# Optimization experiments

Hardware: AMD Instinct MI355X
Metric: run time of the kernel (lower is better)

## Reference

```python
import jax, jax.numpy as jnp
import numpy as np
from jax.tree_util import tree_map

B, T, D = 2, 4096, 1024
C = 512            # chunk_size
P = 16             # n_persistent
H = 2048           # neural-memory hidden
FFN = 4 * D        # ffn_mult * d_model
LR, BETA, ALPHA = 0.01, 0.9, 0.01   # memory lr / momentum / decay
EPS_LN = 1e-5


def _l2norm(x):
    n = jnp.sqrt(jnp.sum(x * x, axis=-1, keepdims=True))
    return x / jnp.maximum(n, 1e-12)


def _ln(x, g, b):
    m = jnp.mean(x, axis=-1, keepdims=True)
    v = jnp.mean((x - m) ** 2, axis=-1, keepdims=True)
    return (x - m) * jax.lax.rsqrt(v + EPS_LN) * g + b


def _mem_mlp(mem, x):
    h = jax.nn.silu(x @ mem['w0'] + mem['b0'])
    return h @ mem['w1'] + mem['b1']


def setup_inputs() -> dict:
    key = jax.random.key(0)
    ks = iter(jax.random.split(key, 32))
    w = lambda *s: jax.random.normal(next(ks), s, jnp.float32) * 0.02
    return dict(
        x=jax.random.normal(next(ks), (B, T, D), jnp.float32),
        wq_ctx=w(D, D), wq=w(D, D), wk=w(D, D), wv=w(D, D),
        w_attn_out=w(D, D), w_gate=w(D, D),
        gate_g=jnp.ones(D), gate_b=jnp.zeros(D),
        n1_g=jnp.ones(D), n1_b=jnp.zeros(D),
        n2_g=jnp.ones(D), n2_b=jnp.zeros(D),
        ffn_w1=w(D, FFN), ffn_b1=jnp.zeros(FFN),
        ffn_w2=w(FFN, D), ffn_b2=jnp.zeros(D),
        pers=w(P, D),
        mem_w0=w(D, H), mem_b0=jnp.zeros(H),
        mem_w1=w(H, D), mem_b1=jnp.zeros(D),
        mem_wk=w(D, D), mem_wv=w(D, D),
    )


def reference(x, wq_ctx, wq, wk, wv, w_attn_out, w_gate, gate_g, gate_b,
              n1_g, n1_b, n2_g, n2_b, ffn_w1, ffn_b1, ffn_w2, ffn_b2,
              pers, mem_w0, mem_b0, mem_w1, mem_b1, mem_wk, mem_wv):
    Bv, Tv, Dv = x.shape
    n_chunks = Tv // C
    scale = Dv ** 0.5
    S = P + 2 * C   # persistent + retrieved-memory tokens + segment
    # prefix-aware causal mask: i attends to j if j < P (persistent prefix) or j <= i
    ii = jnp.arange(S)[:, None]
    jj = jnp.arange(S)[None, :]
    mask = (jj < P) | (jj <= ii)                      # (S, S)

    mem0 = dict(w0=mem_w0, b0=mem_b0, w1=mem_w1, b1=mem_b1)
    mom0 = tree_map(jnp.zeros_like, mem0)

    def attn(seq):                                    # cosine causal attention, single head
        q = _l2norm(seq @ wq) * scale
        k = _l2norm(seq @ wk)
        v = seq @ wv
        scores = jnp.einsum('bqd,bkd->bqk', q, k)
        scores = jnp.where(mask, scores, -jnp.inf)
        a = jax.nn.softmax(scores, axis=-1)
        return jnp.einsum('bqk,bkd->bqd', a, v) @ w_attn_out

    def step(carry, seg):                             # seg: (B, C, D)
        mem, mom = carry
        h = _mem_mlp(mem, _l2norm(seg @ wq_ctx))      # memory retrieval, (B, C, D)
        aug = jnp.concatenate(
            [jnp.broadcast_to(pers, (Bv, P, Dv)), h, seg], axis=1)  # (B, S, D)
        y_aug = aug + attn(_ln(aug, n1_g, n1_b))
        y_t = y_aug[:, P + C:, :]                     # strip persistent, keep last C

        # surprise-gradient memory update with momentum + decay
        kk = y_t @ mem_wk
        vv = y_t @ mem_wv
        loss = lambda m: 0.5 * jnp.sum((_mem_mlp(m, kk) - vv) ** 2) / (Bv * C)
        g = jax.grad(loss)(mem)
        mom = tree_map(lambda m_, g_: BETA * m_ + g_, mom, g)
        mem = tree_map(lambda p_, m_: (1.0 - ALPHA) * p_ - LR * m_, mem, mom)

        mem_out = _mem_mlp(mem, _l2norm(y_t @ wq_ctx))
        gate = jax.nn.sigmoid(_ln(y_t, gate_g, gate_b) @ w_gate)
        o = y_t * gate + mem_out * (1.0 - gate)
        h2 = _ln(o, n2_g, n2_b)
        o = o + (jax.nn.silu(h2 @ ffn_w1 + ffn_b1) @ ffn_w2 + ffn_b2)
        return (mem, mom), o

    x_chunks = x.reshape(Bv, n_chunks, C, Dv).transpose(1, 0, 2, 3)
    _, outs = jax.lax.scan(step, (mem0, mom0), x_chunks)   # (n_chunks, B, C, D)
    return outs.transpose(1, 0, 2, 3).reshape(Bv, Tv, Dv)
```

## Files before the change

### kernel.cpp

```cpp
#include <hip/hip_runtime.h>

#define DD 1024
#define HH 2048
#define TT 4096
#define CC 512
#define PPc 16
#define SB 1040
#define KA 1088
#define FFd 4096
#define NCH 8

typedef _Float16 f16x8 __attribute__((ext_vector_type(8)));
typedef float f32x4 __attribute__((ext_vector_type(4)));

typedef const __attribute__((address_space(1))) _Float16* gas_t;
typedef __attribute__((address_space(3))) _Float16* las_t;

__device__ __forceinline__ void async_cp16(const _Float16* g, _Float16* l) {
    __builtin_amdgcn_global_load_lds((gas_t)g, (las_t)l, 16, 0, 0);
}

template<int N> __device__ __forceinline__ void waitvm() {
    static_assert(N == 0 || N == 2 || N == 3 || N == 4 || N == 6 || N == 8, "unsupported vmcnt");
    if constexpr (N == 0)      asm volatile("s_waitcnt vmcnt(0)" ::: "memory");
    else if constexpr (N == 2) asm volatile("s_waitcnt vmcnt(2)" ::: "memory");
    else if constexpr (N == 3) asm volatile("s_waitcnt vmcnt(3)" ::: "memory");
    else if constexpr (N == 4) asm volatile("s_waitcnt vmcnt(4)" ::: "memory");
    else if constexpr (N == 6) asm volatile("s_waitcnt vmcnt(6)" ::: "memory");
    else                       asm volatile("s_waitcnt vmcnt(8)" ::: "memory");
}
#define BARRIER() asm volatile("s_barrier" ::: "memory")

struct GP {
    const _Float16* A; long bsA;
    const _Float16* Bt; long bsB;
    const float* bias;
    const float* resid; long ldr, bsR;
    const float* aux;   long ldx, bsX;
    float* Cf; long ldc, bsC;
    _Float16* Ch; long ldh, bsH;
    _Float16* Ct; long ldt, bsT;
    float* Mom;
    float* Cf2;
    float s1, s2;
    int M, N, K, act;
};

template<int BM, int BN>
__global__ __launch_bounds__(256) void gemm16(GP g)
{
    constexpr int WM = BM / 2, WN = BN / 2;
    constexpr int FA = WM / 16, FB = WN / 16;
    constexpr int LA = BM / 32, LB = BN / 32;
    constexpr int LL = LA + LB;
    constexpr int APAN = BM * 64, BPAN = BN * 64;
    constexpr int NB = 3;
    __shared__ _Float16 smem[NB * (APAN + BPAN)];
    const int tid = threadIdx.x;

    const int gx = gridDim.x, gy = gridDim.y;
    const int nwg = gx * gy * (int)gridDim.z;
    const int orig = ((int)blockIdx.z * gy + (int)blockIdx.y) * gx + (int)blockIdx.x;
    const int xcd = orig & 7, loc = orig >> 3;
    const int q8 = nwg >> 3, r8 = nwg & 7;
    const int lid = (xcd < r8 ? xcd * (q8 + 1) : r8 * (q8 + 1) + (xcd - r8) * q8) + loc;
    const int bxi = lid % gx;
    const int rem = lid / gx;
    const int byi = rem % gy;
    const int z = rem / gy;

    const int K = g.K;
    const int m0 = byi * BM, n0 = bxi * BN;
    const _Float16* Ab = g.A + (long)z * g.bsA + (long)m0 * K;
    const _Float16* Bb = g.Bt + (long)z * g.bsB + (long)n0 * K;
    const int wave = tid >> 6, lane = tid & 63;
    const int wr = wave >> 1, wc = wave & 1;
    const int fr = lane & 15, kq = lane >> 4;
    const int srow = tid >> 3;
    const int sc8 = (((tid & 7) ^ (srow & 7)) << 3);
    f32x4 acc[FA][FB] = {};

    auto stage = [&](int q, int kk) {
#pragma unroll
        for (int r = 0; r < LA; ++r)
            async_cp16(Ab + (long)(r * 32 + srow) * K + kk + sc8,
                       &smem[q * APAN + r * 2048 + wave * 512]);
#pragma unroll
        for (int r = 0; r < LB; ++r)
            async_cp16(Bb + (long)(r * 32 + srow) * K + kk + sc8,
                       &smem[NB * APAN + q * BPAN + r * 2048 + wave * 512]);
    };

    const int sl0 = ((kq ^ (fr & 7)) << 3);
    const int sl1 = (((4 + kq) ^ (fr & 7)) << 3);

    auto compute = [&](int q) {
        f16x8 af[2][FA], bf[2][FB];
        const int abase = q * APAN;
#pragma unroll
        for (int i = 0; i < FA; ++i) {
            const int ro = (wr * WM + i * 16 + fr) * 64;
            af[0][i] = *(const f16x8*)&smem[abase + ro + sl0];
            af[1][i] = *(const f16x8*)&smem[abase + ro + sl1];
        }
        const int bbase = NB * APAN + q * BPAN;
#pragma unroll
        for (int j = 0; j < FB; ++j) {
            const int ro = (wc * WN + j * 16 + fr) * 64;
            bf[0][j] = *(const f16x8*)&smem[bbase + ro + sl0];
            bf[1][j] = *(const f16x8*)&smem[bbase + ro + sl1];
        }
        __builtin_amdgcn_s_setprio(1);
#pragma unroll
        for (int h = 0; h < 2; ++h)
#pragma unroll
            for (int i = 0; i < FA; ++i)
#pragma unroll
                for (int j = 0; j < FB; ++j)
                    acc[i][j] = __builtin_amdgcn_mfma_f32_16x16x32_f16(af[h][i], bf[h][j], acc[i][j], 0, 0, 0);
        __builtin_amdgcn_s_setprio(0);
    };

    const int nk = K >> 6;
    stage(0, 0); stage(1, 64);
    int qc = 0, qs = 2;
    for (int t = 0; t < nk; ++t) {
        if (t + 1 < nk) waitvm<LL>(); else waitvm<0>();
        BARRIER();
        if (t + 2 < nk) stage(qs, (t + 2) << 6);
        compute(qc);
        qc = (qc == NB - 1) ? 0 : qc + 1;
        qs = (qs == NB - 1) ? 0 : qs + 1;
    }

#pragma unroll
    for (int i = 0; i < FA; ++i) {
        const int gm0 = m0 + wr * WM + i * 16 + kq * 4;
#pragma unroll
        for (int j = 0; j < FB; ++j) {
            const int gn = n0 + wc * WN + j * 16 + fr;
            if (gn >= g.N) continue;
            if (g.act == 4) {
                const int seg = gn >> 10, gl = gn & 1023;
#pragma unroll
                for (int r = 0; r < 4; ++r) {
                    const int gm = gm0 + r;
                    if (gm >= g.M) continue;
                    const float v = acc[i][j][r];
                    if (seg == 0) g.Ch[(long)gm * 1024 + gl] = (_Float16)v;
                    else if (seg == 1) g.Cf[(long)gm * 1024 + gl] = v;
                    else g.Cf2[(long)gm * 1024 + gl] = v;
                }
            } else {
                const float bv = g.bias ? g.bias[gn] : 0.f;
#pragma unroll
                for (int r = 0; r < 4; ++r) {
                    const int gm = gm0 + r;
                    if (gm >= g.M) continue;
                    const float raw = acc[i][j][r] + bv;
                    float av = raw;
                    if (g.act == 1) av = raw / (1.f + __expf(-raw));
                    else if (g.act == 2) {
                        const float a = g.aux[(long)z * g.bsX + (long)gm * g.ldx + gn];
                        const float s = 1.f / (1.f + __expf(-a));
                        av = raw * (s * (1.f + a * (1.f - s)));
                    }
                    float v = g.s1 * av;
                    if (g.resid) v += g.s2 * g.resid[(long)z * g.bsR + (long)gm * g.ldr + gn];
                    if (g.Cf) g.Cf[(long)z * g.bsC + (long)gm * g.ldc + gn] = (g.act == 1) ? raw : v;
                    if (g.Ch) g.Ch[(long)z * g.bsH + (long)gm * g.ldh + gn] = (_Float16)v;
                    acc[i][j][r] = v;
                }
            }
        }
    }

    if (g.Ct && (g.act != 4 || n0 < 1024)) {
        constexpr int TP = BM + 8;
        __syncthreads();
#pragma unroll
        for (int i = 0; i < FA; ++i) {
            const int lm = wr * WM + i * 16 + kq * 4;
#pragma unroll
            for (int j = 0; j < FB; ++j) {
                const int ln = wc * WN + j * 16 + fr;
#pragma unroll
                for (int r = 0; r < 4; ++r)
                    smem[ln * TP + lm + r] = (_Float16)acc[i][j][r];
            }
        }
        __syncthreads();
        constexpr int TPC = 256 / BN;
        constexpr int SEG = BM / TPC;
        const int ln = tid / TPC, part = tid % TPC;
        const int gn = n0 + ln;
        if (gn < g.N) {
            const int gmb = m0 + part * SEG;
            _Float16* dst = g.Ct + (long)z * g.bsT + (long)gn * g.ldt + gmb;
            const _Float16* src = &smem[ln * TP + part * SEG];
#pragma unroll
            for (int gi = 0; gi < SEG / 8; ++gi)
                if (gmb + gi * 8 < g.M)
                    *(uint4*)(dst + gi * 8) = *(const uint4*)(src + gi * 8);
        }
    }
}

__global__ void momupT_k(const float* __restrict__ dW1, float* __restrict__ mom1,
                         float* __restrict__ w1m, _Float16* __restrict__ w1row,
                         _Float16* __restrict__ w1t,
                         const float* __restrict__ dW0, float* __restrict__ mom0,
                         float* __restrict__ w0m, _Float16* __restrict__ w0t)
{
    __shared__ _Float16 t[64][65];
    const int b = blockIdx.x;
    const int tid = threadIdx.x;
    const float* dW; float* mom; float* wm; _Float16* wrow; _Float16* wT;
    int C, RT, r0, c0;
    if (b < 512) {
        dW = dW1; mom = mom1; wm = w1m; wrow = w1row; wT = w1t;
        C = 1024; RT = 2048;
        r0 = (b >> 4) << 6; c0 = (b & 15) << 6;
    } else {
        const int bb = b - 512;
        dW = dW0; mom = mom0; wm = w0m; wrow = nullptr; wT = w0t;
        C = 2048; RT = 1024;
        r0 = (bb >> 5) << 6; c0 = (bb & 31) << 6;
    }
#pragma unroll
    for (int i = 0; i < 4; ++i) {
        const int f = i * 256 + tid;
        const int rr = f >> 4;
        const int c4 = (f & 15) << 2;
        const long idx = (long)(r0 + rr) * C + c0 + c4;
        const float4 d = *(const float4*)(dW + idx);
        float4 mo = *(const float4*)(mom + idx);
        float4 w  = *(const float4*)(wm + idx);
        mo.x = 0.9f * mo.x + d.x; mo.y = 0.9f * mo.y + d.y;
        mo.z = 0.9f * mo.z + d.z; mo.w = 0.9f * mo.w + d.w;
        w.x = 0.99f * w.x - 0.01f * mo.x; w.y = 0.99f * w.y - 0.01f * mo.y;
        w.z = 0.99f * w.z - 0.01f * mo.z; w.w = 0.99f * w.w - 0.01f * mo.w;
        *(float4*)(mom + idx) = mo;
        *(float4*)(wm + idx) = w;
        const _Float16 h0 = (_Float16)w.x, h1 = (_Float16)w.y,
                       h2 = (_Float16)w.z, h3 = (_Float16)w.w;
        if (wrow) {
            wrow[idx] = h0; wrow[idx + 1] = h1;
            wrow[idx + 2] = h2; wrow[idx + 3] = h3;
        }
        t[rr][c4] = h0; t[rr][c4 + 1] = h1; t[rr][c4 + 2] = h2; t[rr][c4 + 3] = h3;
    }
    __syncthreads();
#pragma unroll
    for (int i = 0; i < 4; ++i) {
        const int f = i * 256 + tid;
        const int cc = f >> 4;
        const int rr4 = (f & 15) << 2;
        ushort4 u;
        u.x = *(const unsigned short*)&t[rr4][cc];
        u.y = *(const unsigned short*)&t[rr4 + 1][cc];
        u.z = *(const unsigned short*)&t[rr4 + 2][cc];
        u.w = *(const unsigned short*)&t[rr4 + 3][cc];
        *(ushort4*)(wT + (long)(c0 + cc) * RT + r0 + rr4) = u;
    }
}

__global__ void cvt_k(const float* __restrict__ in, _Float16* __restrict__ out, long n)
{
    long i = ((long)blockIdx.x * 256 + threadIdx.x) * 4;
    if (i >= n) return;
    const float4 v = *(const float4*)(in + i);
    out[i] = (_Float16)v.x; out[i + 1] = (_Float16)v.y;
    out[i + 2] = (_Float16)v.z; out[i + 3] = (_Float16)v.w;
}

__global__ void cvtT_k(const float* __restrict__ in, _Float16* __restrict__ out, int R, int C)
{
    __shared__ _Float16 t[64][65];
    const int c0 = blockIdx.x * 64, r0 = blockIdx.y * 64;
    const int tid = threadIdx.x;
    for (int i = 0; i < 16; ++i) {
        const int lin = i * 256 + tid;
        const int r = lin >> 6, cc = lin & 63;
        t[r][cc] = (_Float16)in[(long)(r0 + r) * C + c0 + cc];
    }
    __syncthreads();
    for (int i = 0; i < 16; ++i) {
        const int lin = i * 256 + tid;
        const int r2 = lin >> 6, c2 = lin & 63;
        out[(long)(c0 + r2) * R + r0 + c2] = t[c2][r2];
    }
}

__global__ void l2n16s_k(const float* __restrict__ in, long ld,
                         _Float16* __restrict__ out, float scale)
{
    const long row = blockIdx.x;
    const float* p = in + row * ld;
    _Float16* q = out + row * DD;
    const int t = threadIdx.x;
    float e0 = p[t], e1 = p[t + 256], e2 = p[t + 512], e3 = p[t + 768];
    __shared__ float rq[256];
    rq[t] = e0 * e0 + e1 * e1 + e2 * e2 + e3 * e3;
    __syncthreads();
    for (int k = 128; k; k >>= 1) { if (t < k) rq[t] += rq[t + k]; __syncthreads(); }
    const float f = scale / fmaxf(sqrtf(rq[0]), 1e-12f);
    q[t] = (_Float16)(e0 * f); q[t + 256] = (_Float16)(e1 * f);
    q[t + 512] = (_Float16)(e2 * f); q[t + 768] = (_Float16)(e3 * f);
}

__global__ void l2qk_k(const float* __restrict__ qk, _Float16* __restrict__ q16,
                       _Float16* __restrict__ k16)
{
    const int blk = blockIdx.x;
    const float* p; _Float16* o; float scale;
    if (blk < 1024) {
        const int b = blk >> 9, r = blk & 511;
        p = qk + (long)(b * SB + PPc + CC + r) * 2048;
        o = q16 + (long)blk * DD; scale = 32.f;
    } else {
        const int row = blk - 1024;
        p = qk + (long)row * 2048 + 1024;
        o = k16 + (long)row * DD; scale = 1.f;
    }
    const int t = threadIdx.x;
    float e0 = p[t], e1 = p[t + 256], e2 = p[t + 512], e3 = p[t + 768];
    __shared__ float rq[256];
    rq[t] = e0 * e0 + e1 * e1 + e2 * e2 + e3 * e3;
    __syncthreads();
    for (int k = 128; k; k >>= 1) { if (t < k) rq[t] += rq[t + k]; __syncthreads(); }
    const float f = scale / fmaxf(sqrtf(rq[0]), 1e-12f);
    o[t] = (_Float16)(e0 * f); o[t + 256] = (_Float16)(e1 * f);
    o[t + 512] = (_Float16)(e2 * f); o[t + 768] = (_Float16)(e3 * f);
}

__global__ void ln16_k(const float* __restrict__ x, const float* __restrict__ g,
                       const float* __restrict__ b, _Float16* __restrict__ o)
{
    const long row = blockIdx.x;
    const float* p = x + row * DD;
    _Float16* q = o + row * DD;
    const int t = threadIdx.x;
    float e0 = p[t], e1 = p[t + 256], e2 = p[t + 512], e3 = p[t + 768];
    __shared__ float rs[256], rq[256];
    rs[t] = e0 + e1 + e2 + e3;
    rq[t] = e0 * e0 + e1 * e1 + e2 * e2 + e3 * e3;
    __syncthreads();
    for (int k = 128; k; k >>= 1) {
        if (t < k) { rs[t] += rs[t + k]; rq[t] += rq[t + k]; }
        __syncthreads();
    }
    const float mean = rs[0] * (1.f / DD);
    const float inv = rsqrtf(rq[0] * (1.f / DD) - mean * mean + 1e-5f);
    q[t]       = (_Float16)((e0 - mean) * inv * g[t]       + b[t]);
    q[t + 256] = (_Float16)((e1 - mean) * inv * g[t + 256] + b[t + 256]);
    q[t + 512] = (_Float16)((e2 - mean) * inv * g[t + 512] + b[t + 512]);
    q[t + 768] = (_Float16)((e3 - mean) * inv * g[t + 768] + b[t + 768]);
}

__global__ void lnaug_k(const float* __restrict__ x, const float* __restrict__ pers,
                        const float* __restrict__ h, const float* __restrict__ g,
                        const float* __restrict__ b, _Float16* __restrict__ out, int c)
{
    const int row = blockIdx.x;
    const int bb = row / SB, i = row % SB;
    const float* p;
    if (i < PPc) p = pers + (long)i * DD;
    else if (i < PPc + CC) p = h + (long)(bb * CC + i - PPc) * DD;
    else p = x + (long)(bb * TT + c * CC + (i - PPc - CC)) * DD;
    _Float16* q = out + (long)row * DD;
    const int t = threadIdx.x;
    float e0 = p[t], e1 = p[t + 256], e2 = p[t + 512], e3 = p[t + 768];
    __shared__ float rs[256], rq[256];
    rs[t] = e0 + e1 + e2 + e3;
    rq[t] = e0 * e0 + e1 * e1 + e2 * e2 + e3 * e3;
    __syncthreads();
    for (int k = 128; k; k >>= 1) {
        if (t < k) { rs[t] += rs[t + k]; rq[t] += rq[t + k]; }
        __syncthreads();
    }
    const float mean = rs[0] * (1.f / DD);
    const float inv = rsqrtf(rq[0] * (1.f / DD) - mean * mean + 1e-5f);
    q[t]       = (_Float16)((e0 - mean) * inv * g[t]       + b[t]);
    q[t + 256] = (_Float16)((e1 - mean) * inv * g[t + 256] + b[t + 256]);
    q[t + 512] = (_Float16)((e2 - mean) * inv * g[t + 512] + b[t + 512]);
    q[t + 768] = (_Float16)((e3 - mean) * inv * g[t + 768] + b[t + 768]);
}

__global__ void softmax16_k(const float* __restrict__ sc, _Float16* __restrict__ pr)
{
    const int blk = blockIdx.x;
    const int r = blk & 511;
    const int i = PPc + CC + r;
    const float* p = sc + (long)blk * SB;
    _Float16* q = pr + (long)blk * KA;
    const int t = threadIdx.x;
    __shared__ float red[256];
    float mx = -3.0e38f;
    for (int j = t; j < SB; j += 256)
        if (j <= i) mx = fmaxf(mx, p[j]);
    red[t] = mx; __syncthreads();
    for (int k = 128; k; k >>= 1) { if (t < k) red[t] = fmaxf(red[t], red[t + k]); __syncthreads(); }
    mx = red[0]; __syncthreads();
    float sum = 0.f;
    for (int j = t; j < SB; j += 256)
        if (j <= i) sum += __expf(p[j] - mx);
    red[t] = sum; __syncthreads();
    for (int k = 128; k; k >>= 1) { if (t < k) red[t] += red[t + k]; __syncthreads(); }
    const float inv = 1.f / red[0];
    for (int j = t; j < KA; j += 256) {
        float e = 0.f;
        if (j < SB && j <= i) e = __expf(p[j] - mx) * inv;
        q[j] = (_Float16)e;
    }
}

__global__ void gateln2_k(const float* __restrict__ yt, const float* __restrict__ gp,
                          const float* __restrict__ mo, const float* __restrict__ g,
                          const float* __restrict__ b, float* __restrict__ OF,
                          _Float16* __restrict__ o16)
{
    const long row = blockIdx.x;
    const int t = threadIdx.x;
    float e[4];
    __shared__ float rs[256], rq[256];
    float ssum = 0.f, qsum = 0.f;
#pragma unroll
    for (int k = 0; k < 4; ++k) {
        const long idx = row * DD + t + k * 256;
        const float s = 1.f / (1.f + __expf(-gp[idx]));
        e[k] = yt[idx] * s + mo[idx] * (1.f - s);
        OF[idx] = e[k];
        ssum += e[k]; qsum += e[k] * e[k];
    }
    rs[t] = ssum; rq[t] = qsum;
    __syncthreads();
    for (int k = 128; k; k >>= 1) {
        if (t < k) { rs[t] += rs[t + k]; rq[t] += rq[t + k]; }
        __syncthreads();
    }
    const float mean = rs[0] * (1.f / DD);
    const float inv = rsqrtf(rq[0] * (1.f / DD) - mean * mean + 1e-5f);
#pragma unroll
    for (int k = 0; k < 4; ++k) {
        const int cc = t + k * 256;
        o16[row * DD + cc] = (_Float16)((e[k] - mean) * inv * g[cc] + b[cc]);
    }
}

__global__ void rowsum2_k(const _Float16* __restrict__ rT, const _Float16* __restrict__ daT,
                          float* __restrict__ db1, float* __restrict__ db0)
{
    const int blk = blockIdx.x;
    const _Float16* p; float* o;
    if (blk < 1024) { p = rT + (long)blk * 1024; o = db1 + blk; }
    else { p = daT + (long)(blk - 1024) * 1024; o = db0 + (blk - 1024); }
    const int t = threadIdx.x;
    __shared__ float red[256];
    red[t] = (float)p[t] + (float)p[t + 256] + (float)p[t + 512] + (float)p[t + 768];
    __syncthreads();
    for (int k = 128; k; k >>= 1) { if (t < k) red[t] += red[t + k]; __syncthreads(); }
    if (t == 0) *o = red[0];
}

__global__ void biasup_k(float* __restrict__ mb0, float* __restrict__ mob0,
                         const float* __restrict__ db0,
                         float* __restrict__ mb1, float* __restrict__ mob1,
                         const float* __restrict__ db1)
{
    const int i = blockIdx.x * 256 + threadIdx.x;
    if (i < HH) {
        const float m = 0.9f * mob0[i] + db0[i];
        mob0[i] = m;
        mb0[i] = 0.99f * mb0[i] - 0.01f * m;
    } else {
        const int j = i - HH;
        if (j < DD) {
            const float m = 0.9f * mob1[j] + db1[j];
            mob1[j] = m;
            mb1[j] = 0.99f * mb1[j] - 0.01f * m;
        }
    }
}

__global__ void zero_k(float* __restrict__ p, long n)
{
    long i = (long)blockIdx.x * 256 + threadIdx.x;
    const long st = (long)gridDim.x * 256;
    for (; i < n; i += st) p[i] = 0.f;
}

extern "C" void kernel_launch(void* const* d_in, const int* in_sizes, int n_in,
                              void* d_out, int out_size, void* d_ws, size_t ws_size,
                              hipStream_t stream)
{
    const float* x          = (const float*)d_in[0];
    const float* wq_ctx     = (const float*)d_in[1];
    const float* wq         = (const float*)d_in[2];
    const float* wk         = (const float*)d_in[3];
    const float* wv         = (const float*)d_in[4];
    const float* w_attn_out = (const float*)d_in[5];
    const float* w_gate     = (const float*)d_in[6];
    const float* gate_g     = (const float*)d_in[7];
    const float* gate_b     = (const float*)d_in[8];
    const float* n1_g       = (const float*)d_in[9];
    const float* n1_b       = (const float*)d_in[10];
    const float* n2_g       = (const float*)d_in[11];
    const float* n2_b       = (const float*)d_in[12];
    const float* ffn_w1     = (const float*)d_in[13];
    const float* ffn_b1     = (const float*)d_in[14];
    const float* ffn_w2     = (const float*)d_in[15];
    const float* ffn_b2     = (const float*)d_in[16];
    const float* pers       = (const float*)d_in[17];
    const float* mem_w0_in  = (const float*)d_in[18];
    const float* mem_b0_in  = (const float*)d_in[19];
    const float* mem_w1_in  = (const float*)d_in[20];
    const float* mem_b1_in  = (const float*)d_in[21];
    const float* mem_wk     = (const float*)d_in[22];
    const float* mem_wv     = (const float*)d_in[23];
    float* out = (float*)d_out;
    (void)in_sizes; (void)n_in; (void)out_size; (void)ws_size;

    char* cur = (char*)d_ws;
    auto allocF = [&](size_t n) { float* p = (float*)cur; cur += n * 4; return p; };
    auto allocH = [&](size_t n) { _Float16* p = (_Float16*)cur; cur += n * 2; return p; };

    float* mw0   = allocF((size_t)DD * HH);
    float* mw1   = allocF((size_t)HH * DD);
    float* mb0   = allocF(HH);
    float* mb1   = allocF(DD);
    float* mom   = allocF((size_t)DD * HH * 2 + HH + DD);
    float* mom_w0 = mom, *mom_w1 = mom + (size_t)DD * HH;
    float* mom_b0 = mom_w1 + (size_t)HH * DD, *mom_b1 = mom_b0 + HH;
    float* F32A  = allocF((size_t)1024 * DD);
    float* F32B  = allocF((size_t)1024 * DD);
    float* F32C  = allocF((size_t)1024 * HH);
    float* F32QK = allocF((size_t)2112 * 2048);
    float* YTF   = allocF((size_t)1024 * DD);
    float* OF    = allocF((size_t)1024 * DD);
    float* db0   = allocF(HH);
    float* db1   = allocF(DD);

    _Float16* x16    = allocH((size_t)2 * TT * DD);
    _Float16* wqcT   = allocH((size_t)DD * DD);
    _Float16* wqkT   = allocH((size_t)2048 * DD);
    _Float16* wvT    = allocH((size_t)DD * DD);
    _Float16* waoT   = allocH((size_t)DD * DD);
    _Float16* wgT    = allocH((size_t)DD * DD);
    _Float16* wmixT  = allocH((size_t)3072 * DD);
    _Float16* f1T    = allocH((size_t)FFd * DD);
    _Float16* f2T    = allocH((size_t)DD * FFd);
    _Float16* w0T    = allocH((size_t)HH * DD);
    _Float16* w1T    = allocH((size_t)DD * HH);
    _Float16* w1p    = allocH((size_t)HH * DD);
    _Float16* xn16   = allocH((size_t)1024 * DD);
    _Float16* h116   = allocH((size_t)1024 * HH);
    _Float16* laug16 = allocH((size_t)2208 * DD);
    _Float16* q16    = allocH((size_t)1024 * DD);
    _Float16* k16    = allocH((size_t)2208 * DD);
    _Float16* vT16   = allocH((size_t)2 * DD * KA);
    _Float16* pr16   = allocH((size_t)2 * 512 * KA);
    _Float16* ao16   = allocH((size_t)1024 * DD);
    _Float16* yt16   = allocH((size_t)1024 * DD);
    _Float16* kk16   = allocH((size_t)1024 * DD);
    _Float16* kkT16  = allocH((size_t)DD * 1024);
    _Float16* hs16   = allocH((size_t)1024 * HH);
    _Float16* hsT16  = allocH((size_t)HH * 1024);
    _Float16* r16    = allocH((size_t)1024 * DD);
    _Float16* rT16   = allocH((size_t)DD * 1024);
    _Float16* da0T   = allocH((size_t)HH * 1024);
    _Float16* qm16   = allocH((size_t)1024 * DD);
    _Float16* a216   = allocH((size_t)1024 * HH);
    _Float16* gl16   = allocH((size_t)1024 * DD);
    _Float16* h216   = allocH((size_t)1024 * DD);
    _Float16* f116   = allocH((size_t)1024 * FFd);

    auto launch = [&](int nz, const GP& g) {
        dim3 grid((g.N + 63) / 64, (g.M + 63) / 64, nz);
        gemm16<64, 64><<<grid, 256, 0, stream>>>(g);
    };

    hipMemcpyAsync(mw0, mem_w0_in, sizeof(float) * DD * HH, hipMemcpyDeviceToDevice, stream);
    hipMemcpyAsync(mw1, mem_w1_in, sizeof(float) * HH * DD, hipMemcpyDeviceToDevice, stream);
    hipMemcpyAsync(mb0, mem_b0_in, sizeof(float) * HH, hipMemcpyDeviceToDevice, stream);
    hipMemcpyAsync(mb1, mem_b1_in, sizeof(float) * DD, hipMemcpyDeviceToDevice, stream);
    zero_k<<<4096, 256, 0, stream>>>(mom, (long)DD * HH * 2 + HH + DD);
    cvt_k<<<(2 * TT * DD) / 1024, 256, 0, stream>>>(x, x16, (long)2 * TT * DD);
    auto T64 = [&](const float* in, _Float16* o, int R, int C) {
        cvtT_k<<<dim3(C / 64, R / 64), 256, 0, stream>>>(in, o, R, C);
    };
    T64(wq_ctx, wqcT, DD, DD);
    T64(wq, wqkT, DD, DD); T64(wk, wqkT + (size_t)1024 * DD, DD, DD);
    T64(wv, wvT, DD, DD); T64(w_attn_out, waoT, DD, DD); T64(w_gate, wgT, DD, DD);
    T64(mem_wk, wmixT, DD, DD); T64(mem_wv, wmixT + (size_t)1024 * DD, DD, DD);
    T64(wq_ctx, wmixT + (size_t)2048 * DD, DD, DD);
    T64(ffn_w1, f1T, DD, FFd); T64(ffn_w2, f2T, FFd, DD);
    T64(mem_w0_in, w0T, DD, HH); T64(mem_w1_in, w1T, HH, DD);
    cvt_k<<<(HH * DD) / 1024, 256, 0, stream>>>(mem_w1_in, w1p, (long)HH * DD);

    for (int c = 0; c < NCH; ++c) {
        GP g;
        g = GP{}; g.A = x16 + (long)c * CC * DD; g.bsA = (long)TT * DD; g.Bt = wqcT;
        g.Cf = F32A; g.ldc = DD; g.bsC = (long)CC * DD;
        g.s1 = 1.f; g.M = CC; g.N = DD; g.K = DD;
        launch(2, g);
        l2n16s_k<<<1024, 256, 0, stream>>>(F32A, DD, xn16, 1.f);
        g = GP{}; g.A = xn16; g.Bt = w0T; g.bias = mb0; g.Ch = h116; g.ldh = HH;
        g.s1 = 1.f; g.M = 1024; g.N = HH; g.K = DD; g.act = 1;
        launch(1, g);
        g = GP{}; g.A = h116; g.Bt = w1T; g.bias = mb1; g.Cf = F32B; g.ldc = DD;
        g.s1 = 1.f; g.M = 1024; g.N = DD; g.K = HH;
        launch(1, g);
        lnaug_k<<<2 * SB, 256, 0, stream>>>(x, pers, F32B, n1_g, n1_b, laug16, c);
        g = GP{}; g.A = laug16; g.Bt = wqkT; g.Cf = F32QK; g.ldc = 2048;
        g.s1 = 1.f; g.M = 2 * SB; g.N = 2048; g.K = DD;
        launch(1, g);
        l2qk_k<<<3104, 256, 0, stream>>>(F32QK, q16, k16);
        g = GP{}; g.A = laug16; g.bsA = (long)SB * DD; g.Bt = wvT;
        g.Ct = vT16; g.ldt = KA; g.bsT = (long)DD * KA;
        g.s1 = 1.f; g.M = SB; g.N = DD; g.K = DD;
        launch(2, g);
        g = GP{}; g.A = q16; g.bsA = (long)512 * DD; g.Bt = k16; g.bsB = (long)SB * DD;
        g.Cf = F32C; g.ldc = SB; g.bsC = (long)512 * SB;
        g.s1 = 1.f; g.M = 512; g.N = SB; g.K = DD;
        launch(2, g);
        softmax16_k<<<1024, 256, 0, stream>>>(F32C, pr16);
        g = GP{}; g.A = pr16; g.bsA = (long)512 * KA; g.Bt = vT16; g.bsB = (long)DD * KA;
        g.Ch = ao16; g.ldh = DD; g.bsH = (long)512 * DD;
        g.s1 = 1.f; g.M = 512; g.N = DD; g.K = KA;
        launch(2, g);
        g = GP{}; g.A = ao16; g.bsA = (long)512 * DD; g.Bt = waoT;
        g.resid = x + (long)c * CC * DD; g.ldr = DD; g.bsR = (long)TT * DD;
        g.Cf = YTF; g.ldc = DD; g.bsC = (long)512 * DD;
        g.Ch = yt16; g.ldh = DD; g.bsH = (long)512 * DD;
        g.s1 = 1.f; g.s2 = 1.f; g.M = 512; g.N = DD; g.K = DD;
        launch(2, g);
        g = GP{}; g.A = yt16; g.Bt = wmixT; g.Ch = kk16; g.Ct = kkT16; g.ldt = 1024;
        g.Cf = F32B; g.Cf2 = F32A;
        g.s1 = 1.f; g.M = 1024; g.N = 3072; g.K = DD; g.act = 4;
        launch(1, g);
        g = GP{}; g.A = kk16; g.Bt = w0T; g.bias = mb0; g.Cf = F32C; g.ldc = HH;
        g.Ch = hs16; g.ldh = HH; g.Ct = hsT16; g.ldt = 1024;
        g.s1 = 1.f; g.M = 1024; g.N = HH; g.K = DD; g.act = 1;
        launch(1, g);
        g = GP{}; g.A = hs16; g.Bt = w1T; g.bias = mb1;
        g.resid = F32B; g.ldr = DD;
        g.Ch = r16; g.ldh = DD; g.Ct = rT16; g.ldt = 1024;
        g.s1 = 1.f / 1024.f; g.s2 = -1.f / 1024.f; g.M = 1024; g.N = DD; g.K = HH;
        launch(1, g);
        g = GP{}; g.A = r16; g.Bt = w1p; g.aux = F32C; g.ldx = HH;
        g.Ct = da0T; g.ldt = 1024;
        g.s1 = 1.f; g.M = 1024; g.N = HH; g.K = DD; g.act = 2;
        launch(1, g);
        rowsum2_k<<<3072, 256, 0, stream>>>(rT16, da0T, db1, db0);
        g = GP{}; g.A = hsT16; g.Bt = rT16; g.Cf = F32C; g.ldc = DD;
        g.s1 = 1.f; g.M = HH; g.N = DD; g.K = 1024;
        launch(1, g);
        g = GP{}; g.A = kkT16; g.Bt = da0T; g.Cf = F32QK; g.ldc = HH;
        g.s1 = 1.f; g.M = DD; g.N = HH; g.K = 1024;
        launch(1, g);
        momupT_k<<<1024, 256, 0, stream>>>(F32C, mom_w1, mw1, w1p, w1T,
                                           F32QK, mom_w0, mw0, w0T);
        biasup_k<<<12, 256, 0, stream>>>(mb0, mom_b0, db0, mb1, mom_b1, db1);
        l2n16s_k<<<1024, 256, 0, stream>>>(F32A, DD, qm16, 1.f);
        g = GP{}; g.A = qm16; g.Bt = w0T; g.bias = mb0; g.Ch = a216; g.ldh = HH;
        g.s1 = 1.f; g.M = 1024; g.N = HH; g.K = DD; g.act = 1;
        launch(1, g);
        g = GP{}; g.A = a216; g.Bt = w1T; g.bias = mb1; g.Cf = F32B; g.ldc = DD;
        g.s1 = 1.f; g.M = 1024; g.N = DD; g.K = HH;
        launch(1, g);
        ln16_k<<<1024, 256, 0, stream>>>(YTF, gate_g, gate_b, gl16);
        g = GP{}; g.A = gl16; g.Bt = wgT; g.Cf = F32C; g.ldc = DD;
        g.s1 = 1.f; g.M = 1024; g.N = DD; g.K = DD;
        launch(1, g);
        gateln2_k<<<1024, 256, 0, stream>>>(YTF, F32C, F32B, n2_g, n2_b, OF, h216);
        g = GP{}; g.A = h216; g.Bt = f1T; g.bias = ffn_b1; g.Ch = f116; g.ldh = FFd;
        g.s1 = 1.f; g.M = 1024; g.N = FFd; g.K = DD; g.act = 1;
        launch(1, g);
        g = GP{}; g.A = f116; g.bsA = (long)512 * FFd; g.Bt = f2T; g.bias = ffn_b2;
        g.resid = OF; g.ldr = DD; g.bsR = (long)512 * DD;
        g.Cf = out + (long)c * CC * DD; g.ldc = DD; g.bsC = (long)TT * DD;
        g.s1 = 1.f; g.s2 = 1.f; g.M = 512; g.N = DD; g.K = FFd;
        launch(2, g);
    }
}
```

Measured before the change: 3.125 ms.

## Deepen GEMM LDS pipeline to four stages and fuse tail elementwise kernels

The GEMM kernel's shared-memory ring goes from three to four buffers, so three K-slices are prefetched ahead of the compute stage, with the vmcnt waits adjusted to match. Separately, the bias row-sum, bias momentum update, L2-normalisation of the retrieval query and the gate LayerNorm are merged into one launch, removing three kernel launches per chunk. The deeper ring uses more LDS per block, which may lower occupancy for the larger tiles. The fused kernel moves the gate LN and query normalisation earlier in the stream, which assumes YTF and F32A are already final at that point.

```diff
diff --git a/kernel.cpp b/kernel.cpp
--- a/kernel.cpp
+++ b/kernel.cpp
@@ -54,7 +54,7 @@
     constexpr int LA = BM / 32, LB = BN / 32;
     constexpr int LL = LA + LB;
     constexpr int APAN = BM * 64, BPAN = BN * 64;
-    constexpr int NB = 3;
+    constexpr int NB = 4;
     __shared__ _Float16 smem[NB * (APAN + BPAN)];
     const int tid = threadIdx.x;
 
@@ -122,15 +122,17 @@
     };
 
     const int nk = K >> 6;
-    stage(0, 0); stage(1, 64);
-    int qc = 0, qs = 2;
+    stage(0, 0); stage(1, 64); stage(2, 128);
+    int qc = 0, qs = 3;
     for (int t = 0; t < nk; ++t) {
-        if (t + 1 < nk) waitvm<LL>(); else waitvm<0>();
+        if (t + 2 < nk)      waitvm<2 * LL>();
+        else if (t + 1 < nk) waitvm<LL>();
+        else                 waitvm<0>();
         BARRIER();
-        if (t + 2 < nk) stage(qs, (t + 2) << 6);
+        if (t + 3 < nk) stage(qs, (t + 3) << 6);
         compute(qc);
-        qc = (qc == NB - 1) ? 0 : qc + 1;
-        qs = (qs == NB - 1) ? 0 : qs + 1;
+        qc = (qc + 1) & 3;
+        qs = (qs + 1) & 3;
     }
 
 #pragma unroll
@@ -332,30 +334,6 @@
     const float f = scale / fmaxf(sqrtf(rq[0]), 1e-12f);
     o[t] = (_Float16)(e0 * f); o[t + 256] = (_Float16)(e1 * f);
     o[t + 512] = (_Float16)(e2 * f); o[t + 768] = (_Float16)(e3 * f);
-}
-
-__global__ void ln16_k(const float* __restrict__ x, const float* __restrict__ g,
-                       const float* __restrict__ b, _Float16* __restrict__ o)
-{
-    const long row = blockIdx.x;
-    const float* p = x + row * DD;
-    _Float16* q = o + row * DD;
-    const int t = threadIdx.x;
-    float e0 = p[t], e1 = p[t + 256], e2 = p[t + 512], e3 = p[t + 768];
-    __shared__ float rs[256], rq[256];
-    rs[t] = e0 + e1 + e2 + e3;
-    rq[t] = e0 * e0 + e1 * e1 + e2 * e2 + e3 * e3;
-    __syncthreads();
-    for (int k = 128; k; k >>= 1) {
-        if (t < k) { rs[t] += rs[t + k]; rq[t] += rq[t + k]; }
-        __syncthreads();
-    }
-    const float mean = rs[0] * (1.f / DD);
-    const float inv = rsqrtf(rq[0] * (1.f / DD) - mean * mean + 1e-5f);
-    q[t]       = (_Float16)((e0 - mean) * inv * g[t]       + b[t]);
-    q[t + 256] = (_Float16)((e1 - mean) * inv * g[t + 256] + b[t + 256]);
-    q[t + 512] = (_Float16)((e2 - mean) * inv * g[t + 512] + b[t + 512]);
-    q[t + 768] = (_Float16)((e3 - mean) * inv * g[t + 768] + b[t + 768]);
 }
 
 __global__ void lnaug_k(const float* __restrict__ x, const float* __restrict__ pers,
@@ -448,38 +426,64 @@
     }
 }
 
-__global__ void rowsum2_k(const _Float16* __restrict__ rT, const _Float16* __restrict__ daT,
-                          float* __restrict__ db1, float* __restrict__ db0)
+__global__ void tailfuse_k(const _Float16* __restrict__ rT, const _Float16* __restrict__ daT,
+                           float* __restrict__ mb0, float* __restrict__ mob0,
+                           float* __restrict__ mb1, float* __restrict__ mob1,
+                           const float* __restrict__ qmp, _Float16* __restrict__ qm16,
+                           const float* __restrict__ ytf, const float* __restrict__ gg,
+                           const float* __restrict__ gb, _Float16* __restrict__ gl)
 {
     const int blk = blockIdx.x;
-    const _Float16* p; float* o;
-    if (blk < 1024) { p = rT + (long)blk * 1024; o = db1 + blk; }
-    else { p = daT + (long)(blk - 1024) * 1024; o = db0 + (blk - 1024); }
     const int t = threadIdx.x;
-    __shared__ float red[256];
-    red[t] = (float)p[t] + (float)p[t + 256] + (float)p[t + 512] + (float)p[t + 768];
-    __syncthreads();
-    for (int k = 128; k; k >>= 1) { if (t < k) red[t] += red[t + k]; __syncthreads(); }
-    if (t == 0) *o = red[0];
-}
-
-__global__ void biasup_k(float* __restrict__ mb0, float* __restrict__ mob0,
-                         const float* __restrict__ db0,
-                         float* __restrict__ mb1, float* __restrict__ mob1,
-                         const float* __restrict__ db1)
-{
-    const int i = blockIdx.x * 256 + threadIdx.x;
-    if (i < HH) {
-        const float m = 0.9f * mob0[i] + db0[i];
-        mob0[i] = m;
-        mb0[i] = 0.99f * mb0[i] - 0.01f * m;
+    __shared__ float rs[256], rq[256];
+    if (blk < 3072) {
+        const _Float16* p = (blk < 1024) ? rT + (long)blk * 1024
+                                         : daT + (long)(blk - 1024) * 1024;
+        rs[t] = (float)p[t] + (float)p[t + 256] + (float)p[t + 512] + (float)p[t + 768];
+        __syncthreads();
+        for (int k = 128; k; k >>= 1) { if (t < k) rs[t] += rs[t + k]; __syncthreads(); }
+        if (t == 0) {
+            const float d = rs[0];
+            if (blk < 1024) {
+                const float m = 0.9f * mob1[blk] + d;
+                mob1[blk] = m;
+                mb1[blk] = 0.99f * mb1[blk] - 0.01f * m;
+            } else {
+                const int j = blk - 1024;
+                const float m = 0.9f * mob0[j] + d;
+                mob0[j] = m;
+                mb0[j] = 0.99f * mb0[j] - 0.01f * m;
+            }
+        }
+    } else if (blk < 4096) {
+        const long row = blk - 3072;
+        const float* p = qmp + row * DD;
+        _Float16* q = qm16 + row * DD;
+        float e0 = p[t], e1 = p[t + 256], e2 = p[t + 512], e3 = p[t + 768];
+        rq[t] = e0 * e0 + e1 * e1 + e2 * e2 + e3 * e3;
+        __syncthreads();
+        for (int k = 128; k; k >>= 1) { if (t < k) rq[t] += rq[t + k]; __syncthreads(); }
+        const float f = 1.f / fmaxf(sqrtf(rq[0]), 1e-12f);
+        q[t] = (_Float16)(e0 * f); q[t + 256] = (_Float16)(e1 * f);
+        q[t + 512] = (_Float16)(e2 * f); q[t + 768] = (_Float16)(e3 * f);
     } else {
-        const int j = i - HH;
-        if (j < DD) {
-            const float m = 0.9f * mob1[j] + db1[j];
-            mob1[j] = m;
-            mb1[j] = 0.99f * mb1[j] - 0.01f * m;
-        }
+        const long row = blk - 4096;
+        const float* p = ytf + row * DD;
+        _Float16* q = gl + row * DD;
+        float e0 = p[t], e1 = p[t + 256], e2 = p[t + 512], e3 = p[t + 768];
+        rs[t] = e0 + e1 + e2 + e3;
+        rq[t] = e0 * e0 + e1 * e1 + e2 * e2 + e3 * e3;
+        __syncthreads();
+        for (int k = 128; k; k >>= 1) {
+            if (t < k) { rs[t] += rs[t + k]; rq[t] += rq[t + k]; }
+            __syncthreads();
+        }
+        const float mean = rs[0] * (1.f / DD);
+        const float inv = rsqrtf(rq[0] * (1.f / DD) - mean * mean + 1e-5f);
+        q[t]       = (_Float16)((e0 - mean) * inv * gg[t]       + gb[t]);
+        q[t + 256] = (_Float16)((e1 - mean) * inv * gg[t + 256] + gb[t + 256]);
+        q[t + 512] = (_Float16)((e2 - mean) * inv * gg[t + 512] + gb[t + 512]);
+        q[t + 768] = (_Float16)((e3 - mean) * inv * gg[t + 768] + gb[t + 768]);
     }
 }
 
@@ -538,8 +542,6 @@
     float* F32QK = allocF((size_t)2112 * 2048);
     float* YTF   = allocF((size_t)1024 * DD);
     float* OF    = allocF((size_t)1024 * DD);
-    float* db0   = allocF(HH);
-    float* db1   = allocF(DD);
 
     _Float16* x16    = allocH((size_t)2 * TT * DD);
     _Float16* wqcT   = allocH((size_t)DD * DD);
@@ -652,7 +654,8 @@
         g.Ct = da0T; g.ldt = 1024;
         g.s1 = 1.f; g.M = 1024; g.N = HH; g.K = DD; g.act = 2;
         launch(1, g);
-        rowsum2_k<<<3072, 256, 0, stream>>>(rT16, da0T, db1, db0);
+        tailfuse_k<<<5120, 256, 0, stream>>>(rT16, da0T, mb0, mom_b0, mb1, mom_b1,
+                                             F32A, qm16, YTF, gate_g, gate_b, gl16);
         g = GP{}; g.A = hsT16; g.Bt = rT16; g.Cf = F32C; g.ldc = DD;
         g.s1 = 1.f; g.M = HH; g.N = DD; g.K = 1024;
         launch(1, g);
@@ -661,15 +664,12 @@
         launch(1, g);
         momupT_k<<<1024, 256, 0, stream>>>(F32C, mom_w1, mw1, w1p, w1T,
                                            F32QK, mom_w0, mw0, w0T);
-        biasup_k<<<12, 256, 0, stream>>>(mb0, mom_b0, db0, mb1, mom_b1, db1);
-        l2n16s_k<<<1024, 256, 0, stream>>>(F32A, DD, qm16, 1.f);
         g = GP{}; g.A = qm16; g.Bt = w0T; g.bias = mb0; g.Ch = a216; g.ldh = HH;
         g.s1 = 1.f; g.M = 1024; g.N = HH; g.K = DD; g.act = 1;
         launch(1, g);
         g = GP{}; g.A = a216; g.Bt = w1T; g.bias = mb1; g.Cf = F32B; g.ldc = DD;
         g.s1 = 1.f; g.M = 1024; g.N = DD; g.K = HH;
         launch(1, g);
-        ln16_k<<<1024, 256, 0, stream>>>(YTF, gate_g, gate_b, gl16);
         g = GP{}; g.A = gl16; g.Bt = wgT; g.Cf = F32C; g.ldc = DD;
         g.s1 = 1.f; g.M = 1024; g.N = DD; g.K = DD;
         launch(1, g);
```

Result: slower. 3.272 ms (+4.7%).
